# Optimization experiments

Hardware: AMD Instinct MI355X
Metric: run time of the kernel (lower is better)

Reference implementation:

```python
import jax, jax.numpy as jnp
import numpy as np

TEMPERATURE = 0.2
EPS = 1e-12


def setup_inputs() -> dict:
    key = jax.random.key(0)
    k1, k2 = jax.random.split(key)
    x = jax.random.normal(k1, (262144, 256), dtype=jnp.float32)
    protos = jax.random.normal(k2, (512, 256), dtype=jnp.float32)
    # buffer is initialized as F.normalize(randn, dim=1)
    protos = protos / jnp.sqrt(jnp.sum(protos * protos, axis=-1, keepdims=True) + EPS)
    return {"x": x, "prototypes": protos, "k": 5}


def reference(x, prototypes, k):
    # L2-normalize inputs (F.normalize p=2 along last dim)
    xn = x / jnp.maximum(jnp.sqrt(jnp.sum(x * x, axis=-1, keepdims=True)), EPS)
    # cosine similarity against prototypes: (B, P)
    sims = jnp.einsum('bd,pd->bp', xn, prototypes)
    # top-k selection over prototypes
    topk_vals, topk_idx = jax.lax.top_k(sims, k)          # (B, k)
    # temperature-scaled softmax over the k winners
    topk_sm = jax.nn.softmax(topk_vals / TEMPERATURE, axis=-1)
    # scatter into sparse activation (B, P)
    B = sims.shape[0]
    rows = jnp.arange(B)[:, None]
    sparse_act = jnp.zeros_like(sims).at[rows, topk_idx].set(topk_sm)
    return sparse_act
```

## Files before the change

kernel.cpp:

```cpp
#include <hip/hip_runtime.h>
#include <math.h>

#define DIM   256
#define NP    512
#define RB    32
#define NT    256
#define PITCH 260
#define CAND_CAP 16
#define KSEL  5

typedef float f32x4 __attribute__((ext_vector_type(4)));
typedef short short8 __attribute__((ext_vector_type(8)));

__device__ __forceinline__ unsigned short f32_to_bf16_rne(float f) {
    unsigned u = __float_as_uint(f);
    u += 0x7FFFu + ((u >> 16) & 1u);
    return (unsigned short)(u >> 16);
}

__global__ __launch_bounds__(256) void protos_pack(const float* __restrict__ protos,
                                                   unsigned short* __restrict__ pbf) {
    int t  = blockIdx.x * 256 + threadIdx.x;
    int dd = t & 7;
    int m  = (t >> 3) & 15;
    int kq = (t >> 7) & 3;
    int ks = (t >> 9) & 7;
    int pg = t >> 12;
    float v = protos[(pg * 16 + m) * DIM + ks * 32 + kq * 8 + dd];
    pbf[t] = (unsigned short)(__float_as_uint(v) >> 16);
}

__global__ __launch_bounds__(NT, 4) void hub_kernel(
    const float* __restrict__ x,
    const float* __restrict__ protos,
    const unsigned short* __restrict__ pbf,
    float* __restrict__ out)
{
    __shared__ float          xs[RB * PITCH];
    __shared__ float          nrm[RB];
    __shared__ unsigned int   ktop[RB][2][KSEL];
    __shared__ unsigned int   u5[RB];
    __shared__ int            scnt[RB];
    __shared__ unsigned short cidx[RB][CAND_CAP];
    __shared__ float          cval[RB][CAND_CAP];
    __shared__ float          top5v[RB][KSEL];
    __shared__ int            top5i[RB][KSEL];

    const int tid  = threadIdx.x;
    const int wave = tid >> 6;
    const int lane = tid & 63;
    const size_t r0 = (size_t)blockIdx.x * RB;

    {
        const float4* xg = (const float4*)(x + r0 * DIM);
        #pragma unroll
        for (int i = 0; i < 8; ++i) {
            int fi = tid + i * NT;
            int r = fi >> 6, c4 = fi & 63;
            *(float4*)(&xs[r * PITCH + c4 * 4]) = xg[fi];
        }
        if (tid < RB) scnt[tid] = 0;
    }
    __syncthreads();

    #pragma unroll
    for (int rr = 0; rr < 8; ++rr) {
        int r = wave * 8 + rr;
        double sq = 0.0;
        #pragma unroll
        for (int j = 0; j < 4; ++j) { double xv = (double)xs[r * PITCH + lane * 4 + j]; sq += xv * xv; }
        #pragma unroll
        for (int s = 32; s > 0; s >>= 1) sq += __shfl_xor(sq, s);
        if (lane == 0) nrm[r] = fmaxf(sqrtf((float)sq), 1e-12f);
    }
    __syncthreads();

    #pragma unroll
    for (int i = 0; i < 32; ++i) {
        int idx = tid + i * NT;
        int r = idx >> 8, d = idx & 255;
        xs[r * PITCH + d] = xs[r * PITCH + d] / nrm[r];
    }
    __syncthreads();

    const int half   = wave >> 1;
    const int rbase  = (wave & 1) * 16;
    const int mylane = lane & 15;
    const int kq     = lane >> 4;
    const int g      = lane >> 4;

    const short8* __restrict__ pbf8 = (const short8*)pbf;
    f32x4 acc[16];
    #pragma unroll
    for (int t2 = 0; t2 < 16; ++t2) acc[t2] = (f32x4)(0.0f);

    #pragma unroll
    for (int ks = 0; ks < 8; ++ks) {
        const float* src = &xs[(rbase + mylane) * PITCH + ks * 32 + kq * 8];
        float4 f0 = *(const float4*)(src);
        float4 f1 = *(const float4*)(src + 4);
        short8 a;
        a[0] = (short)f32_to_bf16_rne(f0.x); a[1] = (short)f32_to_bf16_rne(f0.y);
        a[2] = (short)f32_to_bf16_rne(f0.z); a[3] = (short)f32_to_bf16_rne(f0.w);
        a[4] = (short)f32_to_bf16_rne(f1.x); a[5] = (short)f32_to_bf16_rne(f1.y);
        a[6] = (short)f32_to_bf16_rne(f1.z); a[7] = (short)f32_to_bf16_rne(f1.w);
        #pragma unroll
        for (int t2 = 0; t2 < 16; ++t2) {
            short8 b = pbf8[((half * 16 + t2) * 8 + ks) * 64 + lane];
            acc[t2] = __builtin_amdgcn_mfma_f32_16x16x32_bf16(a, b, acc[t2], 0, 0, 0);
        }
    }

    #pragma unroll
    for (int m = 0; m < 4; ++m) {
        unsigned keys[16];
        #pragma unroll
        for (int t2 = 0; t2 < 16; ++t2) {
            unsigned u = __float_as_uint(fmaf(acc[t2][m], 0.25f, 1.5f));
            keys[t2] = (u & 0xFFFFFE00u) | (unsigned)(half * 256 + t2 * 16 + mylane);
        }
        #pragma unroll
        for (int it = 0; it < KSEL; ++it) {
            unsigned loc = 0;
            #pragma unroll
            for (int t2 = 0; t2 < 16; ++t2) loc = keys[t2] > loc ? keys[t2] : loc;
            #pragma unroll
            for (int s = 1; s < 16; s <<= 1) {
                unsigned o = (unsigned)__shfl_xor((int)loc, s);
                loc = o > loc ? o : loc;
            }
            if (mylane == 0) ktop[rbase + g * 4 + m][half][it] = loc;
            #pragma unroll
            for (int t2 = 0; t2 < 16; ++t2) keys[t2] = (keys[t2] == loc) ? 0u : keys[t2];
        }
    }
    __syncthreads();

    if (tid < RB) {
        unsigned L[KSEL], R[KSEL];
        #pragma unroll
        for (int j = 0; j < KSEL; ++j) { L[j] = ktop[tid][0][j]; R[j] = ktop[tid][1][j]; }
        int i = 0, j = 0; unsigned last = 0;
        #pragma unroll
        for (int s = 0; s < KSEL; ++s) {
            if (L[i] >= R[j]) last = L[i++]; else last = R[j++];
        }
        u5[tid] = last;
    }
    __syncthreads();

    #pragma unroll
    for (int m = 0; m < 4; ++m) {
        int row = rbase + g * 4 + m;
        unsigned tk = (u5[row] & 0xFFFFFE00u) - 0x1000u;
        #pragma unroll
        for (int t2 = 0; t2 < 16; ++t2) {
            unsigned u = __float_as_uint(fmaf(acc[t2][m], 0.25f, 1.5f)) & 0xFFFFFE00u;
            if (u >= tk) {
                int slot = atomicAdd(&scnt[row], 1);
                if (slot < CAND_CAP) cidx[row][slot] = (unsigned short)(half * 256 + t2 * 16 + mylane);
            }
        }
    }
    __syncthreads();

    {
        int row = tid >> 3;
        int s = tid & 7;
        int n = min(scnt[row], CAND_CAP);
        int i0 = 2 * s, i1 = 2 * s + 1;
        if (i0 < n) {
            int p0 = (int)cidx[row][i0];
            int p1 = (i1 < n) ? (int)cidx[row][i1] : p0;
            const float4* pr0 = (const float4*)(protos + (size_t)p0 * DIM);
            const float4* pr1 = (const float4*)(protos + (size_t)p1 * DIM);
            const float* xr = &xs[row * PITCH];
            float a0 = 0.f, a1 = 0.f;
            #pragma unroll 8
            for (int d4 = 0; d4 < 64; ++d4) {
                float4 xv = *(const float4*)(xr + d4 * 4);
                float4 q0 = pr0[d4];
                float4 q1 = pr1[d4];
                a0 = fmaf(xv.x, q0.x, a0); a0 = fmaf(xv.y, q0.y, a0);
                a0 = fmaf(xv.z, q0.z, a0); a0 = fmaf(xv.w, q0.w, a0);
                a1 = fmaf(xv.x, q1.x, a1); a1 = fmaf(xv.y, q1.y, a1);
                a1 = fmaf(xv.z, q1.z, a1); a1 = fmaf(xv.w, q1.w, a1);
            }
            cval[row][i0] = a0;
            if (i1 < n) cval[row][i1] = a1;
        }
    }
    __syncthreads();

    if (tid < RB) {
        int row = tid;
        int n = min(scnt[row], CAND_CAP);
        float vv[CAND_CAP]; int ii[CAND_CAP];
        #pragma unroll
        for (int j = 0; j < CAND_CAP; ++j) {
            vv[j] = (j < n) ? cval[row][j] : -1e30f;
            ii[j] = (j < n) ? (int)cidx[row][j] : 0x7fffffff;
        }
        float vsel[KSEL]; int isel[KSEL];
        #pragma unroll
        for (int it = 0; it < KSEL; ++it) {
            float bv = -1e30f; int bi = 0x7fffffff;
            #pragma unroll
            for (int j = 0; j < CAND_CAP; ++j)
                if (vv[j] > bv || (vv[j] == bv && ii[j] < bi)) { bv = vv[j]; bi = ii[j]; }
            vsel[it] = bv; isel[it] = bi;
            #pragma unroll
            for (int j = 0; j < CAND_CAP; ++j)
                if (ii[j] == bi) { vv[j] = -1e30f; ii[j] = 0x7fffffff; }
        }
        double z[KSEL];
        #pragma unroll
        for (int it = 0; it < KSEL; ++it) z[it] = (double)(vsel[it] / 0.2f);
        double mm = z[0]; double e[KSEL]; double sum = 0.0;
        #pragma unroll
        for (int it = 0; it < KSEL; ++it) { e[it] = exp(z[it] - mm); sum += e[it]; }
        #pragma unroll
        for (int it = 0; it < KSEL; ++it) {
            top5v[row][it] = (float)(e[it] / sum);
            top5i[row][it] = isel[it];
        }
    }
    __syncthreads();

    float* outb = out + r0 * NP;
    #pragma unroll
    for (int i = 0; i < 16; ++i) {
        int fi = tid + i * NT;
        int r = fi >> 7, c0 = (fi & 127) << 2;
        float4 vvv = make_float4(0.f, 0.f, 0.f, 0.f);
        #pragma unroll
        for (int j = 0; j < KSEL; ++j) {
            int idx = top5i[r][j]; float val = top5v[r][j];
            if (c0     == idx) vvv.x = val;
            if (c0 + 1 == idx) vvv.y = val;
            if (c0 + 2 == idx) vvv.z = val;
            if (c0 + 3 == idx) vvv.w = val;
        }
        ((float4*)outb)[fi] = vvv;
    }
}

extern "C" void kernel_launch(void* const* d_in, const int* in_sizes, int n_in,
                              void* d_out, int out_size, void* d_ws, size_t ws_size,
                              hipStream_t stream) {
    const float* x      = (const float*)d_in[0];
    const float* protos = (const float*)d_in[1];
    float* out = (float*)d_out;
    unsigned short* pbf = (unsigned short*)d_ws;

    hipLaunchKernelGGL(protos_pack, dim3(512), dim3(256), 0, stream, protos, pbf);

    const int rows   = in_sizes[0] / DIM;
    const int blocks = rows / RB;
    hipLaunchKernelGGL(hub_kernel, dim3(blocks), dim3(NT), 0, stream,
                       x, protos, pbf, out);
}
```

Baseline: 645.6 us.

## Halve row block to 16 and split prototypes across four waves

Result: faster. 588.6 us (-8.8%).

```diff
diff --git a/kernel.cpp b/kernel.cpp
--- a/kernel.cpp
+++ b/kernel.cpp
@@ -3,7 +3,7 @@
 
 #define DIM   256
 #define NP    512
-#define RB    32
+#define RB    16
 #define NT    256
 #define PITCH 260
 #define CAND_CAP 16
@@ -30,7 +30,7 @@
     pbf[t] = (unsigned short)(__float_as_uint(v) >> 16);
 }
 
-__global__ __launch_bounds__(NT, 4) void hub_kernel(
+__global__ __launch_bounds__(NT, 6) void hub_kernel(
     const float* __restrict__ x,
     const float* __restrict__ protos,
     const unsigned short* __restrict__ pbf,
@@ -38,13 +38,15 @@
 {
     __shared__ float          xs[RB * PITCH];
     __shared__ float          nrm[RB];
-    __shared__ unsigned int   ktop[RB][2][KSEL];
-    __shared__ unsigned int   u5[RB];
+    __shared__ unsigned       selbuf[RB * 4 * KSEL];
+    __shared__ unsigned       u5[RB];
     __shared__ int            scnt[RB];
     __shared__ unsigned short cidx[RB][CAND_CAP];
-    __shared__ float          cval[RB][CAND_CAP];
     __shared__ float          top5v[RB][KSEL];
     __shared__ int            top5i[RB][KSEL];
+
+    unsigned (*ktop)[4][KSEL] = (unsigned(*)[4][KSEL])selbuf;
+    float    (*cval)[CAND_CAP] = (float(*)[CAND_CAP])selbuf;
 
     const int tid  = threadIdx.x;
     const int wave = tid >> 6;
@@ -54,7 +56,7 @@
     {
         const float4* xg = (const float4*)(x + r0 * DIM);
         #pragma unroll
-        for (int i = 0; i < 8; ++i) {
+        for (int i = 0; i < 4; ++i) {
             int fi = tid + i * NT;
             int r = fi >> 6, c4 = fi & 63;
             *(float4*)(&xs[r * PITCH + c4 * 4]) = xg[fi];
@@ -64,8 +66,8 @@
     __syncthreads();
 
     #pragma unroll
-    for (int rr = 0; rr < 8; ++rr) {
-        int r = wave * 8 + rr;
+    for (int rr = 0; rr < 4; ++rr) {
+        int r = wave * 4 + rr;
         double sq = 0.0;
         #pragma unroll
         for (int j = 0; j < 4; ++j) { double xv = (double)xs[r * PITCH + lane * 4 + j]; sq += xv * xv; }
@@ -76,27 +78,26 @@
     __syncthreads();
 
     #pragma unroll
-    for (int i = 0; i < 32; ++i) {
+    for (int i = 0; i < 16; ++i) {
         int idx = tid + i * NT;
         int r = idx >> 8, d = idx & 255;
         xs[r * PITCH + d] = xs[r * PITCH + d] / nrm[r];
     }
     __syncthreads();
 
-    const int half   = wave >> 1;
-    const int rbase  = (wave & 1) * 16;
+    const int qg     = wave;
     const int mylane = lane & 15;
     const int kq     = lane >> 4;
     const int g      = lane >> 4;
 
     const short8* __restrict__ pbf8 = (const short8*)pbf;
-    f32x4 acc[16];
-    #pragma unroll
-    for (int t2 = 0; t2 < 16; ++t2) acc[t2] = (f32x4)(0.0f);
+    f32x4 acc[8];
+    #pragma unroll
+    for (int t2 = 0; t2 < 8; ++t2) acc[t2] = (f32x4)(0.0f);
 
     #pragma unroll
     for (int ks = 0; ks < 8; ++ks) {
-        const float* src = &xs[(rbase + mylane) * PITCH + ks * 32 + kq * 8];
+        const float* src = &xs[mylane * PITCH + ks * 32 + kq * 8];
         float4 f0 = *(const float4*)(src);
         float4 f1 = *(const float4*)(src + 4);
         short8 a;
@@ -105,89 +106,88 @@
         a[4] = (short)f32_to_bf16_rne(f1.x); a[5] = (short)f32_to_bf16_rne(f1.y);
         a[6] = (short)f32_to_bf16_rne(f1.z); a[7] = (short)f32_to_bf16_rne(f1.w);
         #pragma unroll
-        for (int t2 = 0; t2 < 16; ++t2) {
-            short8 b = pbf8[((half * 16 + t2) * 8 + ks) * 64 + lane];
+        for (int t2 = 0; t2 < 8; ++t2) {
+            short8 b = pbf8[(size_t)qg * 4096 + t2 * 512 + ks * 64 + lane];
             acc[t2] = __builtin_amdgcn_mfma_f32_16x16x32_bf16(a, b, acc[t2], 0, 0, 0);
         }
     }
 
     #pragma unroll
     for (int m = 0; m < 4; ++m) {
-        unsigned keys[16];
-        #pragma unroll
-        for (int t2 = 0; t2 < 16; ++t2) {
+        unsigned keys[8];
+        #pragma unroll
+        for (int t2 = 0; t2 < 8; ++t2) {
             unsigned u = __float_as_uint(fmaf(acc[t2][m], 0.25f, 1.5f));
-            keys[t2] = (u & 0xFFFFFE00u) | (unsigned)(half * 256 + t2 * 16 + mylane);
+            keys[t2] = (u & 0xFFFFFE00u) | (unsigned)(qg * 128 + t2 * 16 + mylane);
         }
         #pragma unroll
         for (int it = 0; it < KSEL; ++it) {
             unsigned loc = 0;
             #pragma unroll
-            for (int t2 = 0; t2 < 16; ++t2) loc = keys[t2] > loc ? keys[t2] : loc;
+            for (int t2 = 0; t2 < 8; ++t2) loc = keys[t2] > loc ? keys[t2] : loc;
             #pragma unroll
             for (int s = 1; s < 16; s <<= 1) {
                 unsigned o = (unsigned)__shfl_xor((int)loc, s);
                 loc = o > loc ? o : loc;
             }
-            if (mylane == 0) ktop[rbase + g * 4 + m][half][it] = loc;
-            #pragma unroll
-            for (int t2 = 0; t2 < 16; ++t2) keys[t2] = (keys[t2] == loc) ? 0u : keys[t2];
+            if (mylane == 0) ktop[g * 4 + m][qg][it] = loc;
+            #pragma unroll
+            for (int t2 = 0; t2 < 8; ++t2) keys[t2] = (keys[t2] == loc) ? 0u : keys[t2];
         }
     }
     __syncthreads();
 
     if (tid < RB) {
-        unsigned L[KSEL], R[KSEL];
-        #pragma unroll
-        for (int j = 0; j < KSEL; ++j) { L[j] = ktop[tid][0][j]; R[j] = ktop[tid][1][j]; }
-        int i = 0, j = 0; unsigned last = 0;
-        #pragma unroll
-        for (int s = 0; s < KSEL; ++s) {
-            if (L[i] >= R[j]) last = L[i++]; else last = R[j++];
-        }
-        u5[tid] = last;
+        unsigned A[KSEL], B[KSEL], M1[KSEL], M2[KSEL];
+        #pragma unroll
+        for (int j = 0; j < KSEL; ++j) { A[j] = ktop[tid][0][j]; B[j] = ktop[tid][1][j]; }
+        { int i = 0, j = 0;
+          #pragma unroll
+          for (int s = 0; s < KSEL; ++s) { M1[s] = (A[i] >= B[j]) ? A[i++] : B[j++]; } }
+        #pragma unroll
+        for (int j = 0; j < KSEL; ++j) { A[j] = ktop[tid][2][j]; B[j] = ktop[tid][3][j]; }
+        { int i = 0, j = 0;
+          #pragma unroll
+          for (int s = 0; s < KSEL; ++s) { M2[s] = (A[i] >= B[j]) ? A[i++] : B[j++]; } }
+        { int i = 0, j = 0; unsigned last = 0;
+          #pragma unroll
+          for (int s = 0; s < KSEL; ++s) { last = (M1[i] >= M2[j]) ? M1[i++] : M2[j++]; }
+          u5[tid] = last; }
     }
     __syncthreads();
 
     #pragma unroll
     for (int m = 0; m < 4; ++m) {
-        int row = rbase + g * 4 + m;
+        int row = g * 4 + m;
         unsigned tk = (u5[row] & 0xFFFFFE00u) - 0x1000u;
         #pragma unroll
-        for (int t2 = 0; t2 < 16; ++t2) {
+        for (int t2 = 0; t2 < 8; ++t2) {
             unsigned u = __float_as_uint(fmaf(acc[t2][m], 0.25f, 1.5f)) & 0xFFFFFE00u;
             if (u >= tk) {
                 int slot = atomicAdd(&scnt[row], 1);
-                if (slot < CAND_CAP) cidx[row][slot] = (unsigned short)(half * 256 + t2 * 16 + mylane);
+                if (slot < CAND_CAP) cidx[row][slot] = (unsigned short)(qg * 128 + t2 * 16 + mylane);
             }
         }
     }
     __syncthreads();
 
     {
-        int row = tid >> 3;
-        int s = tid & 7;
+        int row = tid >> 4;
+        int slot = tid & 15;
         int n = min(scnt[row], CAND_CAP);
-        int i0 = 2 * s, i1 = 2 * s + 1;
-        if (i0 < n) {
-            int p0 = (int)cidx[row][i0];
-            int p1 = (i1 < n) ? (int)cidx[row][i1] : p0;
-            const float4* pr0 = (const float4*)(protos + (size_t)p0 * DIM);
-            const float4* pr1 = (const float4*)(protos + (size_t)p1 * DIM);
+        if (slot < n) {
+            int p = (int)cidx[row][slot];
+            const float4* pr = (const float4*)(protos + (size_t)p * DIM);
             const float* xr = &xs[row * PITCH];
-            float a0 = 0.f, a1 = 0.f;
+            float a0 = 0.f;
             #pragma unroll 8
             for (int d4 = 0; d4 < 64; ++d4) {
                 float4 xv = *(const float4*)(xr + d4 * 4);
-                float4 q0 = pr0[d4];
-                float4 q1 = pr1[d4];
-                a0 = fmaf(xv.x, q0.x, a0); a0 = fmaf(xv.y, q0.y, a0);
-                a0 = fmaf(xv.z, q0.z, a0); a0 = fmaf(xv.w, q0.w, a0);
-                a1 = fmaf(xv.x, q1.x, a1); a1 = fmaf(xv.y, q1.y, a1);
-                a1 = fmaf(xv.z, q1.z, a1); a1 = fmaf(xv.w, q1.w, a1);
+                float4 q = pr[d4];
+                a0 = fmaf(xv.x, q.x, a0); a0 = fmaf(xv.y, q.y, a0);
+                a0 = fmaf(xv.z, q.z, a0); a0 = fmaf(xv.w, q.w, a0);
             }
-            cval[row][i0] = a0;
-            if (i1 < n) cval[row][i1] = a1;
+            cval[row][slot] = a0;
         }
     }
     __syncthreads();
@@ -229,7 +229,7 @@
 
     float* outb = out + r0 * NP;
     #pragma unroll
-    for (int i = 0; i < 16; ++i) {
+    for (int i = 0; i < 8; ++i) {
         int fi = tid + i * NT;
         int r = fi >> 7, c0 = (fi & 127) << 2;
         float4 vvv = make_float4(0.f, 0.f, 0.f, 0.f);
```
